# Kernel optimization log

Measured on AMD Instinct MI355X. Metric: run time of the kernel, lower is better.

Reference implementation:

```python
import jax, jax.numpy as jnp
from jax import lax
import numpy as np

N, T, D, H, HG, OG = 2048, 256, 16, 256, 256, 128

def setup_inputs() -> dict:
    key = jax.random.key(0)
    ks = jax.random.split(key, 16)
    s = 0.05
    return {
        'x':    jax.random.normal(ks[0], (N, T, D), jnp.float32),
        'Wih0': jax.random.normal(ks[1], (4 * H, D), jnp.float32) * s,
        'Whh0': jax.random.normal(ks[2], (4 * H, H), jnp.float32) * s,
        'bih0': jax.random.normal(ks[3], (4 * H,), jnp.float32) * s,
        'bhh0': jax.random.normal(ks[4], (4 * H,), jnp.float32) * s,
        'Wih1': jax.random.normal(ks[5], (4 * H, H), jnp.float32) * s,
        'Whh1': jax.random.normal(ks[6], (4 * H, H), jnp.float32) * s,
        'bih1': jax.random.normal(ks[7], (4 * H,), jnp.float32) * s,
        'bhh1': jax.random.normal(ks[8], (4 * H,), jnp.float32) * s,
        'Wg1':  jax.random.normal(ks[9], (H, HG), jnp.float32) * s,
        'Wg2':  jax.random.normal(ks[10], (HG, OG), jnp.float32) * s,
        'Wfc':  jax.random.normal(ks[11], (OG, 1), jnp.float32) * s,
        'bfc':  jax.random.normal(ks[12], (1,), jnp.float32) * s,
    }

def lstm_layer(x, Wih, Whh, bih, bhh):
    # x: [N, T, Din]; torch gate order i, f, g, o stacked along 4H
    n = x.shape[0]
    h4 = Whh.shape[0]
    hid = h4 // 4
    xg = jnp.einsum('ntd,gd->ntg', x, Wih) + bih + bhh  # precompute input part
    def step(carry, g_t):
        h, c = carry
        g = g_t + h @ Whh.T
        i, f, gg, o = jnp.split(g, 4, axis=-1)
        c = jax.nn.sigmoid(f) * c + jax.nn.sigmoid(i) * jnp.tanh(gg)
        h = jax.nn.sigmoid(o) * jnp.tanh(c)
        return (h, c), h
    h0 = jnp.zeros((n, hid), x.dtype)
    (_, _), hs = lax.scan(step, (h0, h0), jnp.swapaxes(xg, 0, 1))
    return jnp.swapaxes(hs, 0, 1)  # [N, T, H]

def adjacency(nf):
    # detached correlation graph + symmetric degree normalization
    f = lax.stop_gradient(nf)
    xc = f - f.mean(axis=1, keepdims=True)
    cov = xc @ xc.T
    d = jnp.sqrt(jnp.diag(cov))
    corr = jnp.nan_to_num(jnp.clip(cov / (d[:, None] * d[None, :]), -1.0, 1.0))
    A = corr + jnp.eye(f.shape[0], dtype=f.dtype)
    dinv = jnp.power(A.sum(axis=1), -0.5)
    dinv = jnp.where(jnp.isinf(dinv), 0.0, dinv)
    return dinv[:, None] * A * dinv[None, :]

def reference(x, Wih0, Whh0, bih0, bhh0, Wih1, Whh1, bih1, bhh1, Wg1, Wg2, Wfc, bfc):
    h = lstm_layer(x, Wih0, Whh0, bih0, bhh0)
    h = lstm_layer(h, Wih1, Whh1, bih1, bhh1)
    nf = h[:, -1, :]                      # [N, H]
    adj = adjacency(nf)                   # [N, N]
    g1 = jax.nn.relu(adj @ (nf @ Wg1))    # GCN layer 1 (dropout=0, eval)
    g2 = adj @ (g1 @ Wg2)                 # GCN layer 2
    pred = g2 @ Wfc + bfc                 # [N, 1]
    return pred[:, 0]
```

## Files before the change

### kernel.cpp

```cpp
#include <hip/hip_runtime.h>
#include <hip/hip_bf16.h>
#include <cmath>

#define NN 2048
#define TT 256
#define DD 16
#define HH 256
#define NBLK 512

typedef __attribute__((ext_vector_type(8))) short short8;
typedef __attribute__((ext_vector_type(4))) float f32x4;

__device__ __forceinline__ float sigmoidf_(float x){ return 1.0f/(1.0f+expf(-x)); }

__device__ __forceinline__ void glds16(const __hip_bfloat16* g, __hip_bfloat16* l){
  __builtin_amdgcn_global_load_lds(
      (const __attribute__((address_space(1))) void*)g,
      (__attribute__((address_space(3))) void*)l, 16, 0, 0);
}
__device__ __forceinline__ void glds16_dev(const __hip_bfloat16* g, __hip_bfloat16* l){
  __builtin_amdgcn_global_load_lds(
      (const __attribute__((address_space(1))) void*)g,
      (__attribute__((address_space(3))) void*)l, 16, 0, 17);
}

__global__ __launch_bounds__(256) void pack_w2(const float* __restrict__ W,
                                               __hip_bfloat16* __restrict__ P){
  int tid = blockIdx.x*256 + threadIdx.x;
  int r = tid >> 8, k = tid & 255;
  float w = W[tid];
  __hip_bfloat16 h = __float2bfloat16(w);
  __hip_bfloat16 l = __float2bfloat16(w - __bfloat162float(h));
  size_t base = (size_t)r*512;
  P[base + k] = h; P[base + 256 + k] = l;
}
__global__ __launch_bounds__(256) void pack_w0(const float* __restrict__ W,
                                               __hip_bfloat16* __restrict__ P){
  int tid = blockIdx.x*256 + threadIdx.x;
  int r = tid >> 4, k = tid & 15;
  float w = W[tid];
  __hip_bfloat16 h = __float2bfloat16(w);
  __hip_bfloat16 l = __float2bfloat16(w - __bfloat162float(h));
  size_t base = (size_t)r*64;
  P[base + k] = h; P[base + 16 + k] = h; P[base + 32 + k] = l;
  P[base + 48 + k] = __float2bfloat16(0.0f);
}
__global__ __launch_bounds__(256) void pack_x(const float* __restrict__ x,
                                              __hip_bfloat16* __restrict__ Xp){
  int tid = blockIdx.x*256 + threadIdx.x;
  const float* xr = x + (size_t)tid*16;
  __hip_bfloat16* o = Xp + (size_t)tid*64;
  for (int k=0;k<16;k++){
    float v = xr[k];
    __hip_bfloat16 h = __float2bfloat16(v);
    __hip_bfloat16 l = __float2bfloat16(v - __bfloat162float(h));
    o[k] = h; o[16+k] = l; o[32+k] = h; o[48+k] = __float2bfloat16(0.0f);
  }
}
__global__ __launch_bounds__(256) void recon_nf(const __hip_bfloat16* __restrict__ hi,
    const __hip_bfloat16* __restrict__ lo, float* __restrict__ nf){
  int tid = blockIdx.x*256 + threadIdx.x;
  nf[tid] = __bfloat162float(hi[tid]) + __bfloat162float(lo[tid]);
}

__global__ __launch_bounds__(256) void bar_init(unsigned* __restrict__ bar){
  for (int i = threadIdx.x; i < 2048; i += 256) bar[i] = 0u;
}

__device__ __forceinline__ void lean_sync(unsigned* bar, int t, int bid){
  __syncthreads();
  if (threadIdx.x == 0){
    const int x = bid & 7;
    unsigned a = __hip_atomic_fetch_add(bar + x*16, 1u, __ATOMIC_RELAXED,
                                        __HIP_MEMORY_SCOPE_AGENT);
    if (a == (unsigned)(64u*(t+1) - 1u)){
      unsigned g = __hip_atomic_fetch_add(bar + 128, 1u, __ATOMIC_RELAXED,
                                          __HIP_MEMORY_SCOPE_AGENT);
      if (g == (unsigned)(8u*(t+1) - 1u)){
        #pragma unroll
        for (int i=0;i<8;i++)
          __hip_atomic_store(bar + 1536 + i*64, (unsigned)(t+1),
                             __ATOMIC_RELAXED, __HIP_MEMORY_SCOPE_AGENT);
      } else {
        while (__hip_atomic_load(bar + 1536 + x*64, __ATOMIC_RELAXED,
                                 __HIP_MEMORY_SCOPE_AGENT) < (unsigned)(t+1))
          __builtin_amdgcn_s_sleep(4);
      }
    } else {
      while (__hip_atomic_load(bar + 1536 + x*64, __ATOMIC_RELAXED,
                               __HIP_MEMORY_SCOPE_AGENT) < (unsigned)(t+1))
        __builtin_amdgcn_s_sleep(4);
    }
  }
  __syncthreads();
}

__device__ __forceinline__ void mm_merged(
    const __hip_bfloat16* __restrict__ Ahi, const __hip_bfloat16* __restrict__ Alo,
    size_t lda,
    const __hip_bfloat16* __restrict__ Bhi, const __hip_bfloat16* __restrict__ Blo,
    size_t ldb, int Klen,
    int m0, int j0, int wv, int lane, int rr, int sw8, int frow,
    f32x4 (&acc)[2][4],
    __hip_bfloat16* AsH, __hip_bfloat16* AsL,
    __hip_bfloat16* BsH, __hip_bfloat16* BsL)
{
  const size_t arow = (size_t)(m0 + wv*32 + rr)*lda + sw8;
  const size_t brow = (size_t)(wv*256 + j0 + rr)*ldb + sw8;
  for (int kb=0; kb<Klen; kb+=64){
    {
      const __hip_bfloat16* AbH = Ahi + arow + kb;
      __hip_bfloat16* AdH = AsH + (wv*32)*64;
      #pragma unroll
      for (int c2=0;c2<4;c2++) glds16_dev(AbH + (size_t)(c2*8)*lda, AdH + c2*8*64);
      const __hip_bfloat16* AbL = Alo + arow + kb;
      __hip_bfloat16* AdL = AsL + (wv*32)*64;
      #pragma unroll
      for (int c2=0;c2<4;c2++) glds16_dev(AbL + (size_t)(c2*8)*lda, AdL + c2*8*64);
      const __hip_bfloat16* Bb1 = Bhi + brow + kb;
      __hip_bfloat16* Bd1 = BsH + (wv<<4)*64;
      glds16(Bb1, Bd1); glds16(Bb1 + (size_t)8*ldb, Bd1 + 8*64);
      const __hip_bfloat16* Bb2 = Blo + brow + kb;
      __hip_bfloat16* Bd2 = BsL + (wv<<4)*64;
      glds16(Bb2, Bd2); glds16(Bb2 + (size_t)8*ldb, Bd2 + 8*64);
    }
    __syncthreads();
    #pragma unroll
    for (int w2=0; w2<2; ++w2){
      const int sl8 = ((((w2<<2) + (lane>>4)) ^ (lane&7)) << 3);
      short8 ah0 = *(const short8*)&AsH[(wv*32 +      frow)*64 + sl8];
      short8 ah1 = *(const short8*)&AsH[(wv*32 + 16 + frow)*64 + sl8];
      short8 al0 = *(const short8*)&AsL[(wv*32 +      frow)*64 + sl8];
      short8 al1 = *(const short8*)&AsL[(wv*32 + 16 + frow)*64 + sl8];
      #pragma unroll
      for (int g=0; g<4; ++g){
        short8 bh = *(const short8*)&BsH[((g<<4) + frow)*64 + sl8];
        acc[0][g] = __builtin_amdgcn_mfma_f32_16x16x32_bf16(ah0, bh, acc[0][g], 0,0,0);
        acc[1][g] = __builtin_amdgcn_mfma_f32_16x16x32_bf16(ah1, bh, acc[1][g], 0,0,0);
        acc[0][g] = __builtin_amdgcn_mfma_f32_16x16x32_bf16(al0, bh, acc[0][g], 0,0,0);
        acc[1][g] = __builtin_amdgcn_mfma_f32_16x16x32_bf16(al1, bh, acc[1][g], 0,0,0);
        short8 bl = *(const short8*)&BsL[((g<<4) + frow)*64 + sl8];
        acc[0][g] = __builtin_amdgcn_mfma_f32_16x16x32_bf16(ah0, bl, acc[0][g], 0,0,0);
        acc[1][g] = __builtin_amdgcn_mfma_f32_16x16x32_bf16(ah1, bl, acc[1][g], 0,0,0);
      }
    }
    __syncthreads();
  }
}

__device__ __forceinline__ void mm_single64(
    const __hip_bfloat16* __restrict__ A, size_t lda,
    const __hip_bfloat16* __restrict__ B, size_t ldb,
    int m0, int j0, int wv, int lane, int rr, int sw8, int frow,
    f32x4 (&acc)[2][4],
    __hip_bfloat16* As0, __hip_bfloat16* Bh0)
{
  {
    const __hip_bfloat16* Ab = A + (size_t)(m0 + wv*32 + rr)*lda + sw8;
    __hip_bfloat16* Ad = As0 + (wv*32)*64;
    #pragma unroll
    for (int c2=0;c2<4;c2++) glds16(Ab + (size_t)(c2*8)*lda, Ad + c2*8*64);
    const __hip_bfloat16* Bb1 = B + (size_t)(wv*256 + j0 + rr)*ldb + sw8;
    __hip_bfloat16* Bd1 = Bh0 + (wv<<4)*64;
    glds16(Bb1, Bd1); glds16(Bb1 + (size_t)8*ldb, Bd1 + 8*64);
  }
  __syncthreads();
  #pragma unroll
  for (int w2=0; w2<2; ++w2){
    const int sl8 = ((((w2<<2) + (lane>>4)) ^ (lane&7)) << 3);
    short8 a0 = *(const short8*)&As0[(wv*32 +      frow)*64 + sl8];
    short8 a1 = *(const short8*)&As0[(wv*32 + 16 + frow)*64 + sl8];
    #pragma unroll
    for (int g=0; g<4; ++g){
      short8 b1 = *(const short8*)&Bh0[((g<<4) + frow)*64 + sl8];
      acc[0][g] = __builtin_amdgcn_mfma_f32_16x16x32_bf16(a0, b1, acc[0][g], 0,0,0);
      acc[1][g] = __builtin_amdgcn_mfma_f32_16x16x32_bf16(a1, b1, acc[1][g], 0,0,0);
    }
  }
  __syncthreads();
}

__global__ __launch_bounds__(256, 2) void lstm2_all(
    const __hip_bfloat16* __restrict__ Xp,
    const __hip_bfloat16* __restrict__ P0ih,
    const __hip_bfloat16* __restrict__ P0hh,
    const __hip_bfloat16* __restrict__ P1ih,
    const __hip_bfloat16* __restrict__ P1hh,
    const float* __restrict__ bih0, const float* __restrict__ bhh0,
    const float* __restrict__ bih1, const float* __restrict__ bhh1,
    __hip_bfloat16* __restrict__ H0hi0, __hip_bfloat16* __restrict__ H0lo0,
    __hip_bfloat16* __restrict__ H0hi1, __hip_bfloat16* __restrict__ H0lo1,
    __hip_bfloat16* __restrict__ H1hi0, __hip_bfloat16* __restrict__ H1lo0,
    __hip_bfloat16* __restrict__ H1hi1, __hip_bfloat16* __restrict__ H1lo1,
    unsigned* __restrict__ bar)
{
  __shared__ __align__(16) __hip_bfloat16 AsH[128*64];
  __shared__ __align__(16) __hip_bfloat16 AsL[128*64];
  __shared__ __align__(16) __hip_bfloat16 BsH[64*64];
  __shared__ __align__(16) __hip_bfloat16 BsL[64*64];

  const int bid = blockIdx.x;
  const int xcd = bid & 7;
  const int slot = bid >> 3;
  const bool isL0 = xcd < 4;
  const int lg = isL0 ? xcd : (xcd - 4);
  const int jg = ((lg & 1) << 3) + (slot & 7);
  const int mg = ((lg >> 1) << 3) + (slot >> 3);
  const int m0 = mg << 7;
  const int j0 = jg << 4;
  const int lane = threadIdx.x & 63, wv = threadIdx.x >> 6;
  const int rr = lane >> 3;
  const int sw8 = (((lane & 7) ^ rr) << 3);
  const int frow = lane & 15;
  const int odd = frow & 1;

  const int j = j0 + frow;
  const float* bih = isL0 ? bih0 : bih1;
  const float* bhh = isL0 ? bhh0 : bhh1;
  const float b0 = bih[j]        + bhh[j];
  const float b1 = bih[HH + j]   + bhh[HH + j];
  const float b2 = bih[2*HH + j] + bhh[2*HH + j];
  const float b3 = bih[3*HH + j] + bhh[3*HH + j];

  float creg[2][4] = {{0.f,0.f,0.f,0.f},{0.f,0.f,0.f,0.f}};

  for (int t = 0; t <= TT; ++t){
    const int p = t & 1;
    const bool active = isL0 ? (t < TT) : (t >= 1);
    if (active){
      f32x4 acc[2][4] = {};
      const __hip_bfloat16* h0p_hi = p ? H0hi0 : H0hi1;
      const __hip_bfloat16* h0p_lo = p ? H0lo0 : H0lo1;
      if (isL0){
        if (t != 0){
          mm_merged(h0p_hi, h0p_lo, 256, P0hh, P0hh+256, 512, 256,
                    m0, j0, wv, lane, rr, sw8, frow, acc, AsH, AsL, BsH, BsL);
        }
        mm_single64(Xp + (size_t)t*64, (size_t)TT*64, P0ih, 64,
                    m0, j0, wv, lane, rr, sw8, frow, acc, AsH, BsH);
      } else {
        mm_merged(h0p_hi, h0p_lo, 256, P1ih, P1ih+256, 512, 256,
                  m0, j0, wv, lane, rr, sw8, frow, acc, AsH, AsL, BsH, BsL);
        if (t != 1){
          const __hip_bfloat16* h1p_hi = p ? H1hi1 : H1hi0;
          const __hip_bfloat16* h1p_lo = p ? H1lo1 : H1lo0;
          mm_merged(h1p_hi, h1p_lo, 256, P1hh, P1hh+256, 512, 256,
                    m0, j0, wv, lane, rr, sw8, frow, acc, AsH, AsL, BsH, BsL);
        }
      }
      __hip_bfloat16* ohi = isL0 ? (p ? H0hi1 : H0hi0)
                                 : (p ? H1hi0 : H1hi1);
      __hip_bfloat16* olo = isL0 ? (p ? H0lo1 : H0lo0)
                                 : (p ? H1lo0 : H1lo1);
      #pragma unroll
      for (int mt=0; mt<2; ++mt){
        const int mrb = m0 + wv*32 + mt*16 + ((lane>>4)<<2);
        #pragma unroll
        for (int r=0; r<4; ++r){
          float gi = acc[mt][0][r] + b0;
          float gf = acc[mt][1][r] + b1;
          float gg = acc[mt][2][r] + b2;
          float go = acc[mt][3][r] + b3;
          float cn = sigmoidf_(gf)*creg[mt][r] + sigmoidf_(gi)*tanhf(gg);
          creg[mt][r] = cn;
          float hv = sigmoidf_(go)*tanhf(cn);
          __hip_bfloat16 hb = __float2bfloat16(hv);
          __hip_bfloat16 lb = __float2bfloat16(hv - __bfloat162float(hb));
          unsigned hs = (unsigned)*reinterpret_cast<unsigned short*>(&hb);
          unsigned ls = (unsigned)*reinterpret_cast<unsigned short*>(&lb);
          unsigned hp = (unsigned)__shfl_xor((int)hs, 1);
          unsigned lp = (unsigned)__shfl_xor((int)ls, 1);
          const size_t base = (size_t)(mrb + r)*HH + (size_t)(j & ~1);
          if (!odd){
            unsigned v = hs | (hp << 16);
            __hip_atomic_store((unsigned*)(ohi + base), v,
                               __ATOMIC_RELAXED, __HIP_MEMORY_SCOPE_AGENT);
          } else {
            unsigned v = lp | (ls << 16);
            __hip_atomic_store((unsigned*)(olo + base), v,
                               __ATOMIC_RELAXED, __HIP_MEMORY_SCOPE_AGENT);
          }
        }
      }
    }
    if (t < TT) lean_sync(bar, t, bid);
  }
}

__global__ __launch_bounds__(256) void gemm_nn(
    float* __restrict__ C, const float* __restrict__ A, const float* __restrict__ B,
    int K, int lda, int ldb, int ldc, int relu)
{
  __shared__ float As_[16][68];
  __shared__ float Bs_[16][64];
  float acc[4][4] = {};
  const int tx = threadIdx.x;
  const int m0 = blockIdx.y<<6, n0 = blockIdx.x<<6;
  const int am = tx>>2, ak = (tx&3)<<2;
  const int bk = tx>>4, bn = (tx&15)<<2;
  const int mm = (tx>>4)<<2, nc = (tx&15)<<2;
  for (int kb=0; kb<K; kb+=16){
    float4 av = *reinterpret_cast<const float4*>(A + (size_t)(m0+am)*lda + kb + ak);
    As_[ak][am]=av.x; As_[ak+1][am]=av.y; As_[ak+2][am]=av.z; As_[ak+3][am]=av.w;
    *reinterpret_cast<float4*>(&Bs_[bk][bn]) =
      *reinterpret_cast<const float4*>(B + (size_t)(kb+bk)*ldb + n0 + bn);
    __syncthreads();
    #pragma unroll
    for (int k=0;k<16;k++){
      float4 a4 = *reinterpret_cast<const float4*>(&As_[k][mm]);
      float4 b4 = *reinterpret_cast<const float4*>(&Bs_[k][nc]);
      acc[0][0]=fmaf(a4.x,b4.x,acc[0][0]); acc[0][1]=fmaf(a4.x,b4.y,acc[0][1]);
      acc[0][2]=fmaf(a4.x,b4.z,acc[0][2]); acc[0][3]=fmaf(a4.x,b4.w,acc[0][3]);
      acc[1][0]=fmaf(a4.y,b4.x,acc[1][0]); acc[1][1]=fmaf(a4.y,b4.y,acc[1][1]);
      acc[1][2]=fmaf(a4.y,b4.z,acc[1][2]); acc[1][3]=fmaf(a4.y,b4.w,acc[1][3]);
      acc[2][0]=fmaf(a4.z,b4.x,acc[2][0]); acc[2][1]=fmaf(a4.z,b4.y,acc[2][1]);
      acc[2][2]=fmaf(a4.z,b4.z,acc[2][2]); acc[2][3]=fmaf(a4.z,b4.w,acc[2][3]);
      acc[3][0]=fmaf(a4.w,b4.x,acc[3][0]); acc[3][1]=fmaf(a4.w,b4.y,acc[3][1]);
      acc[3][2]=fmaf(a4.w,b4.z,acc[3][2]); acc[3][3]=fmaf(a4.w,b4.w,acc[3][3]);
    }
    __syncthreads();
  }
  #pragma unroll
  for (int r=0;r<4;r++){
    float4 v = make_float4(acc[r][0],acc[r][1],acc[r][2],acc[r][3]);
    if (relu){ v.x=fmaxf(v.x,0.f); v.y=fmaxf(v.y,0.f); v.z=fmaxf(v.z,0.f); v.w=fmaxf(v.w,0.f); }
    *reinterpret_cast<float4*>(C + (size_t)(m0+mm+r)*ldc + n0 + nc) = v;
  }
}

__global__ __launch_bounds__(256) void gemm_nt(
    float* __restrict__ C, const float* __restrict__ A, const float* __restrict__ B,
    int K, int lda, int ldb, int ldc)
{
  __shared__ float As_[16][68];
  __shared__ float Bs_[16][68];
  float acc[4][4] = {};
  const int tx = threadIdx.x;
  const int m0 = blockIdx.y<<6, n0 = blockIdx.x<<6;
  const int am = tx>>2, ak = (tx&3)<<2;
  const int mm = (tx>>4)<<2, nc = (tx&15)<<2;
  for (int kb=0; kb<K; kb+=16){
    float4 av = *reinterpret_cast<const float4*>(A + (size_t)(m0+am)*lda + kb + ak);
    As_[ak][am]=av.x; As_[ak+1][am]=av.y; As_[ak+2][am]=av.z; As_[ak+3][am]=av.w;
    float4 bv = *reinterpret_cast<const float4*>(B + (size_t)(n0+am)*ldb + kb + ak);
    Bs_[ak][am]=bv.x; Bs_[ak+1][am]=bv.y; Bs_[ak+2][am]=bv.z; Bs_[ak+3][am]=bv.w;
    __syncthreads();
    #pragma unroll
    for (int k=0;k<16;k++){
      float4 a4 = *reinterpret_cast<const float4*>(&As_[k][mm]);
      float4 b4 = *reinterpret_cast<const float4*>(&Bs_[k][nc]);
      acc[0][0]=fmaf(a4.x,b4.x,acc[0][0]); acc[0][1]=fmaf(a4.x,b4.y,acc[0][1]);
      acc[0][2]=fmaf(a4.x,b4.z,acc[0][2]); acc[0][3]=fmaf(a4.x,b4.w,acc[0][3]);
      acc[1][0]=fmaf(a4.y,b4.x,acc[1][0]); acc[1][1]=fmaf(a4.y,b4.y,acc[1][1]);
      acc[1][2]=fmaf(a4.y,b4.z,acc[1][2]); acc[1][3]=fmaf(a4.y,b4.w,acc[1][3]);
      acc[2][0]=fmaf(a4.z,b4.x,acc[2][0]); acc[2][1]=fmaf(a4.z,b4.y,acc[2][1]);
      acc[2][2]=fmaf(a4.z,b4.z,acc[2][2]); acc[2][3]=fmaf(a4.z,b4.w,acc[2][3]);
      acc[3][0]=fmaf(a4.w,b4.x,acc[3][0]); acc[3][1]=fmaf(a4.w,b4.y,acc[3][1]);
      acc[3][2]=fmaf(a4.w,b4.z,acc[3][2]); acc[3][3]=fmaf(a4.w,b4.w,acc[3][3]);
    }
    __syncthreads();
  }
  #pragma unroll
  for (int r=0;r<4;r++){
    float4 v = make_float4(acc[r][0],acc[r][1],acc[r][2],acc[r][3]);
    *reinterpret_cast<float4*>(C + (size_t)(m0+mm+r)*ldc + n0 + nc) = v;
  }
}

__global__ __launch_bounds__(256) void rowstat(const float* __restrict__ nf,
    float* __restrict__ xc, float* __restrict__ dvec)
{
  __shared__ float red[256];
  int n = blockIdx.x, tx = threadIdx.x;
  float v = nf[(size_t)n*HH + tx];
  red[tx] = v; __syncthreads();
  for (int s=128; s>0; s>>=1){ if (tx<s) red[tx]+=red[tx+s]; __syncthreads(); }
  float mean = red[0] * (1.0f/HH);
  __syncthreads();
  float d = v - mean;
  xc[(size_t)n*HH + tx] = d;
  red[tx] = d*d; __syncthreads();
  for (int s=128; s>0; s>>=1){ if (tx<s) red[tx]+=red[tx+s]; __syncthreads(); }
  if (tx==0) dvec[n] = sqrtf(red[0]);
}

__global__ __launch_bounds__(256) void rowsum(const float* __restrict__ cov,
    const float* __restrict__ dvec, float* __restrict__ dinv)
{
  __shared__ float red[256];
  int i = blockIdx.x, tx = threadIdx.x;
  float di = dvec[i];
  float s = 0.f;
  for (int jj=tx; jj<NN; jj+=256){
    float r = cov[(size_t)i*NN + jj] / (di * dvec[jj]);
    if (r != r) r = 0.f; else r = fminf(1.f, fmaxf(-1.f, r));
    s += r;
  }
  red[tx]=s; __syncthreads();
  for (int st=128; st>0; st>>=1){ if (tx<st) red[tx]+=red[tx+st]; __syncthreads(); }
  if (tx==0){
    float tot = red[0] + 1.0f;
    float p = powf(tot, -0.5f);
    if (isinf(p)) p = 0.f;
    dinv[i] = p;
  }
}

__global__ __launch_bounds__(256) void adjnorm(float* __restrict__ cov,
    const float* __restrict__ dvec, const float* __restrict__ dinv)
{
  size_t idx = (size_t)blockIdx.x*256 + threadIdx.x;
  int i = (int)(idx >> 11), jj = (int)(idx & (NN-1));
  float r = cov[idx] / (dvec[i]*dvec[jj]);
  if (r != r) r = 0.f; else r = fminf(1.f, fmaxf(-1.f, r));
  if (i==jj) r += 1.f;
  cov[idx] = dinv[i]*r*dinv[jj];
}

__global__ __launch_bounds__(128) void predk(const float* __restrict__ G2,
    const float* __restrict__ Wfc, const float* __restrict__ bfc, float* __restrict__ out)
{
  int n = blockIdx.x, tx = threadIdx.x;
  float v = G2[(size_t)n*128 + tx] * Wfc[tx];
  for (int off=32; off>0; off>>=1) v += __shfl_down(v, off);
  __shared__ float p[2];
  if ((tx&63)==0) p[tx>>6] = v;
  __syncthreads();
  if (tx==0) out[n] = p[0] + p[1] + bfc[0];
}

extern "C" void kernel_launch(void* const* d_in, const int* in_sizes, int n_in,
                              void* d_out, int out_size, void* d_ws, size_t ws_size,
                              hipStream_t stream)
{
  const float* x    = (const float*)d_in[0];
  const float* Wih0 = (const float*)d_in[1];
  const float* Whh0 = (const float*)d_in[2];
  const float* bih0 = (const float*)d_in[3];
  const float* bhh0 = (const float*)d_in[4];
  const float* Wih1 = (const float*)d_in[5];
  const float* Whh1 = (const float*)d_in[6];
  const float* bih1 = (const float*)d_in[7];
  const float* bhh1 = (const float*)d_in[8];
  const float* Wg1  = (const float*)d_in[9];
  const float* Wg2  = (const float*)d_in[10];
  const float* Wfc  = (const float*)d_in[11];
  const float* bfc  = (const float*)d_in[12];
  float* out = (float*)d_out;

  char* w = (char*)d_ws;
  auto alloc = [&](size_t bytes){ char* p = w; w += (bytes + 255) & ~(size_t)255; return p; };
  __hip_bfloat16* Xp   = (__hip_bfloat16*)alloc((size_t)NN*TT*64*2);
  __hip_bfloat16* P0hh = (__hip_bfloat16*)alloc((size_t)1024*512*2);
  __hip_bfloat16* P1ih = (__hip_bfloat16*)alloc((size_t)1024*512*2);
  __hip_bfloat16* P1hh = (__hip_bfloat16*)alloc((size_t)1024*512*2);
  __hip_bfloat16* P0ih = (__hip_bfloat16*)alloc((size_t)1024*64*2);
  __hip_bfloat16 *H0hi[2], *H0lo[2], *H1hi[2], *H1lo[2];
  for (int i=0;i<2;i++){ H0hi[i]=(__hip_bfloat16*)alloc((size_t)NN*HH*2);
                         H0lo[i]=(__hip_bfloat16*)alloc((size_t)NN*HH*2); }
  for (int i=0;i<2;i++){ H1hi[i]=(__hip_bfloat16*)alloc((size_t)NN*HH*2);
                         H1lo[i]=(__hip_bfloat16*)alloc((size_t)NN*HH*2); }
  float* nf   = (float*)alloc((size_t)NN*HH*4);
  float* xc   = (float*)alloc((size_t)NN*HH*4);
  float* cov  = (float*)alloc((size_t)NN*NN*4);
  float* t1   = (float*)alloc((size_t)NN*HH*4);
  float* G1   = (float*)alloc((size_t)NN*HH*4);
  float* t2   = (float*)alloc((size_t)NN*128*4);
  float* G2   = (float*)alloc((size_t)NN*128*4);
  float* dvec = (float*)alloc((size_t)NN*4);
  float* dinv = (float*)alloc((size_t)NN*4);
  unsigned* bar = (unsigned*)alloc(8192);

  hipLaunchKernelGGL(bar_init, dim3(1), dim3(256), 0, stream, bar);
  hipLaunchKernelGGL(pack_w2, dim3(1024), dim3(256), 0, stream, Whh0, P0hh);
  hipLaunchKernelGGL(pack_w2, dim3(1024), dim3(256), 0, stream, Wih1, P1ih);
  hipLaunchKernelGGL(pack_w2, dim3(1024), dim3(256), 0, stream, Whh1, P1hh);
  hipLaunchKernelGGL(pack_w0, dim3(64),   dim3(256), 0, stream, Wih0, P0ih);
  hipLaunchKernelGGL(pack_x,  dim3(2048), dim3(256), 0, stream, x, Xp);

  hipLaunchKernelGGL(lstm2_all, dim3(NBLK), dim3(256), 0, stream,
      Xp, P0ih, P0hh, P1ih, P1hh, bih0, bhh0, bih1, bhh1,
      H0hi[0], H0lo[0], H0hi[1], H0lo[1],
      H1hi[0], H1lo[0], H1hi[1], H1lo[1], bar);

  hipLaunchKernelGGL(recon_nf, dim3(2048), dim3(256), 0, stream, H1hi[1], H1lo[1], nf);

  hipLaunchKernelGGL(rowstat, dim3(NN), dim3(256), 0, stream, nf, xc, dvec);
  hipLaunchKernelGGL(gemm_nt, dim3(NN/64, NN/64), dim3(256), 0, stream,
      cov, xc, xc, HH, HH, HH, NN);
  hipLaunchKernelGGL(rowsum, dim3(NN), dim3(256), 0, stream, cov, dvec, dinv);
  hipLaunchKernelGGL(adjnorm, dim3(NN*NN/256), dim3(256), 0, stream, cov, dvec, dinv);

  hipLaunchKernelGGL(gemm_nn, dim3(HH/64, NN/64), dim3(256), 0, stream,
      t1, nf, Wg1, HH, HH, HH, HH, 0);
  hipLaunchKernelGGL(gemm_nn, dim3(HH/64, NN/64), dim3(256), 0, stream,
      G1, cov, t1, NN, NN, HH, HH, 1);
  hipLaunchKernelGGL(gemm_nn, dim3(128/64, NN/64), dim3(256), 0, stream,
      t2, G1, Wg2, HH, HH, 128, 128, 0);
  hipLaunchKernelGGL(gemm_nn, dim3(128/64, NN/64), dim3(256), 0, stream,
      G2, cov, t2, NN, NN, 128, 128, 0);
  hipLaunchKernelGGL(predk, dim3(NN), dim3(128), 0, stream, G2, Wfc, bfc, out);
}
```

Measured before the change: 4.648 ms.

## Repartition persistent LSTM kernel across 768 blocks with unequal layer tiles

The persistent two-layer LSTM kernel now launches 768 blocks at three per CU instead of 512 at two. Layer-1 blocks, which do two recurrent GEMMs per step, get half the rows of layer-0 blocks so per-step work is more even across the grid barrier. Tiles change from 128 rows × 16 gate columns to 64 or 32 rows × 32 gate columns, so weight slices double while activation slices shrink. The grid barrier threshold is raised to match, and the extra co-resident blocks risk more register and LDS pressure and more barrier traffic.

```diff
diff --git a/kernel.cpp b/kernel.cpp
--- a/kernel.cpp
+++ b/kernel.cpp
@@ -6,7 +6,7 @@
 #define TT 256
 #define DD 16
 #define HH 256
-#define NBLK 512
+#define NBLK 768
 
 typedef __attribute__((ext_vector_type(8))) short short8;
 typedef __attribute__((ext_vector_type(4))) float f32x4;
@@ -73,7 +73,7 @@
     const int x = bid & 7;
     unsigned a = __hip_atomic_fetch_add(bar + x*16, 1u, __ATOMIC_RELAXED,
                                         __HIP_MEMORY_SCOPE_AGENT);
-    if (a == (unsigned)(64u*(t+1) - 1u)){
+    if (a == (unsigned)(96u*(t+1) - 1u)){
       unsigned g = __hip_atomic_fetch_add(bar + 128, 1u, __ATOMIC_RELAXED,
                                           __HIP_MEMORY_SCOPE_AGENT);
       if (g == (unsigned)(8u*(t+1) - 1u)){
@@ -95,92 +95,7 @@
   __syncthreads();
 }
 
-__device__ __forceinline__ void mm_merged(
-    const __hip_bfloat16* __restrict__ Ahi, const __hip_bfloat16* __restrict__ Alo,
-    size_t lda,
-    const __hip_bfloat16* __restrict__ Bhi, const __hip_bfloat16* __restrict__ Blo,
-    size_t ldb, int Klen,
-    int m0, int j0, int wv, int lane, int rr, int sw8, int frow,
-    f32x4 (&acc)[2][4],
-    __hip_bfloat16* AsH, __hip_bfloat16* AsL,
-    __hip_bfloat16* BsH, __hip_bfloat16* BsL)
-{
-  const size_t arow = (size_t)(m0 + wv*32 + rr)*lda + sw8;
-  const size_t brow = (size_t)(wv*256 + j0 + rr)*ldb + sw8;
-  for (int kb=0; kb<Klen; kb+=64){
-    {
-      const __hip_bfloat16* AbH = Ahi + arow + kb;
-      __hip_bfloat16* AdH = AsH + (wv*32)*64;
-      #pragma unroll
-      for (int c2=0;c2<4;c2++) glds16_dev(AbH + (size_t)(c2*8)*lda, AdH + c2*8*64);
-      const __hip_bfloat16* AbL = Alo + arow + kb;
-      __hip_bfloat16* AdL = AsL + (wv*32)*64;
-      #pragma unroll
-      for (int c2=0;c2<4;c2++) glds16_dev(AbL + (size_t)(c2*8)*lda, AdL + c2*8*64);
-      const __hip_bfloat16* Bb1 = Bhi + brow + kb;
-      __hip_bfloat16* Bd1 = BsH + (wv<<4)*64;
-      glds16(Bb1, Bd1); glds16(Bb1 + (size_t)8*ldb, Bd1 + 8*64);
-      const __hip_bfloat16* Bb2 = Blo + brow + kb;
-      __hip_bfloat16* Bd2 = BsL + (wv<<4)*64;
-      glds16(Bb2, Bd2); glds16(Bb2 + (size_t)8*ldb, Bd2 + 8*64);
-    }
-    __syncthreads();
-    #pragma unroll
-    for (int w2=0; w2<2; ++w2){
-      const int sl8 = ((((w2<<2) + (lane>>4)) ^ (lane&7)) << 3);
-      short8 ah0 = *(const short8*)&AsH[(wv*32 +      frow)*64 + sl8];
-      short8 ah1 = *(const short8*)&AsH[(wv*32 + 16 + frow)*64 + sl8];
-      short8 al0 = *(const short8*)&AsL[(wv*32 +      frow)*64 + sl8];
-      short8 al1 = *(const short8*)&AsL[(wv*32 + 16 + frow)*64 + sl8];
-      #pragma unroll
-      for (int g=0; g<4; ++g){
-        short8 bh = *(const short8*)&BsH[((g<<4) + frow)*64 + sl8];
-        acc[0][g] = __builtin_amdgcn_mfma_f32_16x16x32_bf16(ah0, bh, acc[0][g], 0,0,0);
-        acc[1][g] = __builtin_amdgcn_mfma_f32_16x16x32_bf16(ah1, bh, acc[1][g], 0,0,0);
-        acc[0][g] = __builtin_amdgcn_mfma_f32_16x16x32_bf16(al0, bh, acc[0][g], 0,0,0);
-        acc[1][g] = __builtin_amdgcn_mfma_f32_16x16x32_bf16(al1, bh, acc[1][g], 0,0,0);
-        short8 bl = *(const short8*)&BsL[((g<<4) + frow)*64 + sl8];
-        acc[0][g] = __builtin_amdgcn_mfma_f32_16x16x32_bf16(ah0, bl, acc[0][g], 0,0,0);
-        acc[1][g] = __builtin_amdgcn_mfma_f32_16x16x32_bf16(ah1, bl, acc[1][g], 0,0,0);
-      }
-    }
-    __syncthreads();
-  }
-}
-
-__device__ __forceinline__ void mm_single64(
-    const __hip_bfloat16* __restrict__ A, size_t lda,
-    const __hip_bfloat16* __restrict__ B, size_t ldb,
-    int m0, int j0, int wv, int lane, int rr, int sw8, int frow,
-    f32x4 (&acc)[2][4],
-    __hip_bfloat16* As0, __hip_bfloat16* Bh0)
-{
-  {
-    const __hip_bfloat16* Ab = A + (size_t)(m0 + wv*32 + rr)*lda + sw8;
-    __hip_bfloat16* Ad = As0 + (wv*32)*64;
-    #pragma unroll
-    for (int c2=0;c2<4;c2++) glds16(Ab + (size_t)(c2*8)*lda, Ad + c2*8*64);
-    const __hip_bfloat16* Bb1 = B + (size_t)(wv*256 + j0 + rr)*ldb + sw8;
-    __hip_bfloat16* Bd1 = Bh0 + (wv<<4)*64;
-    glds16(Bb1, Bd1); glds16(Bb1 + (size_t)8*ldb, Bd1 + 8*64);
-  }
-  __syncthreads();
-  #pragma unroll
-  for (int w2=0; w2<2; ++w2){
-    const int sl8 = ((((w2<<2) + (lane>>4)) ^ (lane&7)) << 3);
-    short8 a0 = *(const short8*)&As0[(wv*32 +      frow)*64 + sl8];
-    short8 a1 = *(const short8*)&As0[(wv*32 + 16 + frow)*64 + sl8];
-    #pragma unroll
-    for (int g=0; g<4; ++g){
-      short8 b1 = *(const short8*)&Bh0[((g<<4) + frow)*64 + sl8];
-      acc[0][g] = __builtin_amdgcn_mfma_f32_16x16x32_bf16(a0, b1, acc[0][g], 0,0,0);
-      acc[1][g] = __builtin_amdgcn_mfma_f32_16x16x32_bf16(a1, b1, acc[1][g], 0,0,0);
-    }
-  }
-  __syncthreads();
-}
-
-__global__ __launch_bounds__(256, 2) void lstm2_all(
+__global__ __launch_bounds__(256, 3) void lstm2_all(
     const __hip_bfloat16* __restrict__ Xp,
     const __hip_bfloat16* __restrict__ P0ih,
     const __hip_bfloat16* __restrict__ P0hh,
@@ -194,75 +109,184 @@
     __hip_bfloat16* __restrict__ H1hi1, __hip_bfloat16* __restrict__ H1lo1,
     unsigned* __restrict__ bar)
 {
-  __shared__ __align__(16) __hip_bfloat16 AsH[128*64];
-  __shared__ __align__(16) __hip_bfloat16 AsL[128*64];
-  __shared__ __align__(16) __hip_bfloat16 BsH[64*64];
-  __shared__ __align__(16) __hip_bfloat16 BsL[64*64];
+  __shared__ __align__(16) __hip_bfloat16 AsH[64*64];
+  __shared__ __align__(16) __hip_bfloat16 AsL[64*64];
+  __shared__ __align__(16) __hip_bfloat16 BsH[128*64];
+  __shared__ __align__(16) __hip_bfloat16 BsL[128*64];
 
   const int bid = blockIdx.x;
   const int xcd = bid & 7;
   const int slot = bid >> 3;
-  const bool isL0 = xcd < 4;
-  const int lg = isL0 ? xcd : (xcd - 4);
-  const int jg = ((lg & 1) << 3) + (slot & 7);
-  const int mg = ((lg >> 1) << 3) + (slot >> 3);
-  const int m0 = mg << 7;
-  const int j0 = jg << 4;
+  const bool isL0 = slot < 32;
+  const int s = isL0 ? slot : (slot - 32);
+  const int m0 = xcd*256 + (isL0 ? ((s>>3)<<6) : ((s>>3)<<5));
+  const int j0 = (s & 7) << 5;
   const int lane = threadIdx.x & 63, wv = threadIdx.x >> 6;
   const int rr = lane >> 3;
   const int sw8 = (((lane & 7) ^ rr) << 3);
   const int frow = lane & 15;
   const int odd = frow & 1;
-
-  const int j = j0 + frow;
-  const float* bih = isL0 ? bih0 : bih1;
-  const float* bhh = isL0 ? bhh0 : bhh1;
-  const float b0 = bih[j]        + bhh[j];
-  const float b1 = bih[HH + j]   + bhh[HH + j];
-  const float b2 = bih[2*HH + j] + bhh[2*HH + j];
-  const float b3 = bih[3*HH + j] + bhh[3*HH + j];
+  const int jsub = wv & 1;
+  const int wmb = isL0 ? ((wv>>1)<<5) : ((wv>>1)<<4);
+  const int nms = isL0 ? 2 : 1;
+
+  const int j = j0 + (jsub<<4) + frow;
+  const float* bihp = isL0 ? bih0 : bih1;
+  const float* bhhp = isL0 ? bhh0 : bhh1;
+  const float b0 = bihp[j]        + bhhp[j];
+  const float b1 = bihp[HH + j]   + bhhp[HH + j];
+  const float b2 = bihp[2*HH + j] + bhhp[2*HH + j];
+  const float b3 = bihp[3*HH + j] + bhhp[3*HH + j];
 
   float creg[2][4] = {{0.f,0.f,0.f,0.f},{0.f,0.f,0.f,0.f}};
+
+  const size_t aW0 = (size_t)(m0 + wv*16 + rr)*256 + sw8;
+  const size_t aW1 = (size_t)(m0 + wv*8  + rr)*256 + sw8;
+  const size_t bW  = (size_t)(wv*256 + j0 + rr)*512 + sw8;
+  const size_t bxW = (size_t)(wv*256 + j0 + rr)*64  + sw8;
 
   for (int t = 0; t <= TT; ++t){
     const int p = t & 1;
     const bool active = isL0 ? (t < TT) : (t >= 1);
     if (active){
       f32x4 acc[2][4] = {};
-      const __hip_bfloat16* h0p_hi = p ? H0hi0 : H0hi1;
-      const __hip_bfloat16* h0p_lo = p ? H0lo0 : H0lo1;
       if (isL0){
         if (t != 0){
-          mm_merged(h0p_hi, h0p_lo, 256, P0hh, P0hh+256, 512, 256,
-                    m0, j0, wv, lane, rr, sw8, frow, acc, AsH, AsL, BsH, BsL);
+          const __hip_bfloat16* hh = p ? H0hi0 : H0hi1;
+          const __hip_bfloat16* hl = p ? H0lo0 : H0lo1;
+          for (int kb=0; kb<256; kb+=64){
+            glds16_dev(hh + aW0 + kb,                 AsH + (wv*16)*64);
+            glds16_dev(hh + aW0 + (size_t)8*256 + kb, AsH + (wv*16+8)*64);
+            glds16_dev(hl + aW0 + kb,                 AsL + (wv*16)*64);
+            glds16_dev(hl + aW0 + (size_t)8*256 + kb, AsL + (wv*16+8)*64);
+            #pragma unroll
+            for (int c2=0;c2<4;c2++){
+              glds16(P0hh + bW + (size_t)(c2*8)*512 + kb,       BsH + (wv*32 + c2*8)*64);
+              glds16(P0hh + 256 + bW + (size_t)(c2*8)*512 + kb, BsL + (wv*32 + c2*8)*64);
+            }
+            __syncthreads();
+            #pragma unroll
+            for (int w2=0; w2<2; ++w2){
+              const int sl8 = ((((w2<<2) + (lane>>4)) ^ (lane&7)) << 3);
+              #pragma unroll
+              for (int ms=0; ms<2; ++ms){
+                short8 ah = *(const short8*)&AsH[(wmb + ms*16 + frow)*64 + sl8];
+                short8 al = *(const short8*)&AsL[(wmb + ms*16 + frow)*64 + sl8];
+                #pragma unroll
+                for (int g=0; g<4; ++g){
+                  const int brow = (g*32 + (jsub<<4) + frow)*64 + sl8;
+                  short8 bh = *(const short8*)&BsH[brow];
+                  acc[ms][g] = __builtin_amdgcn_mfma_f32_16x16x32_bf16(ah, bh, acc[ms][g], 0,0,0);
+                  acc[ms][g] = __builtin_amdgcn_mfma_f32_16x16x32_bf16(al, bh, acc[ms][g], 0,0,0);
+                  short8 bl = *(const short8*)&BsL[brow];
+                  acc[ms][g] = __builtin_amdgcn_mfma_f32_16x16x32_bf16(ah, bl, acc[ms][g], 0,0,0);
+                }
+              }
+            }
+            __syncthreads();
+          }
         }
-        mm_single64(Xp + (size_t)t*64, (size_t)TT*64, P0ih, 64,
-                    m0, j0, wv, lane, rr, sw8, frow, acc, AsH, BsH);
+        {
+          const size_t axW = (size_t)(m0 + wv*16 + rr)*((size_t)TT*64)
+                           + (size_t)t*64 + sw8;
+          glds16(Xp + axW,                       AsH + (wv*16)*64);
+          glds16(Xp + axW + (size_t)8*TT*64,     AsH + (wv*16+8)*64);
+          #pragma unroll
+          for (int c2=0;c2<4;c2++)
+            glds16(P0ih + bxW + (size_t)(c2*8)*64, BsH + (wv*32 + c2*8)*64);
+          __syncthreads();
+          #pragma unroll
+          for (int w2=0; w2<2; ++w2){
+            const int sl8 = ((((w2<<2) + (lane>>4)) ^ (lane&7)) << 3);
+            #pragma unroll
+            for (int ms=0; ms<2; ++ms){
+              short8 a0 = *(const short8*)&AsH[(wmb + ms*16 + frow)*64 + sl8];
+              #pragma unroll
+              for (int g=0; g<4; ++g){
+                short8 b1v = *(const short8*)&BsH[(g*32 + (jsub<<4) + frow)*64 + sl8];
+                acc[ms][g] = __builtin_amdgcn_mfma_f32_16x16x32_bf16(a0, b1v, acc[ms][g], 0,0,0);
+              }
+            }
+          }
+          __syncthreads();
+        }
       } else {
-        mm_merged(h0p_hi, h0p_lo, 256, P1ih, P1ih+256, 512, 256,
-                  m0, j0, wv, lane, rr, sw8, frow, acc, AsH, AsL, BsH, BsL);
-        if (t != 1){
-          const __hip_bfloat16* h1p_hi = p ? H1hi1 : H1hi0;
-          const __hip_bfloat16* h1p_lo = p ? H1lo1 : H1lo0;
-          mm_merged(h1p_hi, h1p_lo, 256, P1hh, P1hh+256, 512, 256,
-                    m0, j0, wv, lane, rr, sw8, frow, acc, AsH, AsL, BsH, BsL);
+        const __hip_bfloat16* h0h = p ? H0hi0 : H0hi1;
+        const __hip_bfloat16* h0l = p ? H0lo0 : H0lo1;
+        for (int kb=0; kb<256; kb+=64){
+          glds16_dev(h0h + aW1 + kb, AsH + (wv*8)*64);
+          glds16_dev(h0l + aW1 + kb, AsL + (wv*8)*64);
+          #pragma unroll
+          for (int c2=0;c2<4;c2++){
+            glds16(P1ih + bW + (size_t)(c2*8)*512 + kb,       BsH + (wv*32 + c2*8)*64);
+            glds16(P1ih + 256 + bW + (size_t)(c2*8)*512 + kb, BsL + (wv*32 + c2*8)*64);
+          }
+          __syncthreads();
+          #pragma unroll
+          for (int w2=0; w2<2; ++w2){
+            const int sl8 = ((((w2<<2) + (lane>>4)) ^ (lane&7)) << 3);
+            short8 ah = *(const short8*)&AsH[(wmb + frow)*64 + sl8];
+            short8 al = *(const short8*)&AsL[(wmb + frow)*64 + sl8];
+            #pragma unroll
+            for (int g=0; g<4; ++g){
+              const int brow = (g*32 + (jsub<<4) + frow)*64 + sl8;
+              short8 bh = *(const short8*)&BsH[brow];
+              acc[0][g] = __builtin_amdgcn_mfma_f32_16x16x32_bf16(ah, bh, acc[0][g], 0,0,0);
+              acc[0][g] = __builtin_amdgcn_mfma_f32_16x16x32_bf16(al, bh, acc[0][g], 0,0,0);
+              short8 bl = *(const short8*)&BsL[brow];
+              acc[0][g] = __builtin_amdgcn_mfma_f32_16x16x32_bf16(ah, bl, acc[0][g], 0,0,0);
+            }
+          }
+          __syncthreads();
+        }
+        if (t >= 2){
+          const __hip_bfloat16* h1h = p ? H1hi1 : H1hi0;
+          const __hip_bfloat16* h1l = p ? H1lo1 : H1lo0;
+          for (int kb=0; kb<256; kb+=64){
+            glds16_dev(h1h + aW1 + kb, AsH + (wv*8)*64);
+            glds16_dev(h1l + aW1 + kb, AsL + (wv*8)*64);
+            #pragma unroll
+            for (int c2=0;c2<4;c2++){
+              glds16(P1hh + bW + (size_t)(c2*8)*512 + kb,       BsH + (wv*32 + c2*8)*64);
+              glds16(P1hh + 256 + bW + (size_t)(c2*8)*512 + kb, BsL + (wv*32 + c2*8)*64);
+            }
+            __syncthreads();
+            #pragma unroll
+            for (int w2=0; w2<2; ++w2){
+              const int sl8 = ((((w2<<2) + (lane>>4)) ^ (lane&7)) << 3);
+              short8 ah = *(const short8*)&AsH[(wmb + frow)*64 + sl8];
+              short8 al = *(const short8*)&AsL[(wmb + frow)*64 + sl8];
+              #pragma unroll
+              for (int g=0; g<4; ++g){
+                const int brow = (g*32 + (jsub<<4) + frow)*64 + sl8;
+                short8 bh = *(const short8*)&BsH[brow];
+                acc[0][g] = __builtin_amdgcn_mfma_f32_16x16x32_bf16(ah, bh, acc[0][g], 0,0,0);
+                acc[0][g] = __builtin_amdgcn_mfma_f32_16x16x32_bf16(al, bh, acc[0][g], 0,0,0);
+                short8 bl = *(const short8*)&BsL[brow];
+                acc[0][g] = __builtin_amdgcn_mfma_f32_16x16x32_bf16(ah, bl, acc[0][g], 0,0,0);
+              }
+            }
+            __syncthreads();
+          }
         }
       }
+
       __hip_bfloat16* ohi = isL0 ? (p ? H0hi1 : H0hi0)
                                  : (p ? H1hi0 : H1hi1);
       __hip_bfloat16* olo = isL0 ? (p ? H0lo1 : H0lo0)
                                  : (p ? H1lo0 : H1lo1);
-      #pragma unroll
-      for (int mt=0; mt<2; ++mt){
-        const int mrb = m0 + wv*32 + mt*16 + ((lane>>4)<<2);
+      float* cr = creg[0];
+      for (int ms=0; ms<nms; ++ms){
+        const int mrb = m0 + wmb + ms*16 + ((lane>>4)<<2);
+        float* cm = (ms==0) ? creg[0] : creg[1];
         #pragma unroll
         for (int r=0; r<4; ++r){
-          float gi = acc[mt][0][r] + b0;
-          float gf = acc[mt][1][r] + b1;
-          float gg = acc[mt][2][r] + b2;
-          float go = acc[mt][3][r] + b3;
-          float cn = sigmoidf_(gf)*creg[mt][r] + sigmoidf_(gi)*tanhf(gg);
-          creg[mt][r] = cn;
+          float gi = acc[ms][0][r] + b0;
+          float gf = acc[ms][1][r] + b1;
+          float gg = acc[ms][2][r] + b2;
+          float go = acc[ms][3][r] + b3;
+          float cn = sigmoidf_(gf)*cm[r] + sigmoidf_(gi)*tanhf(gg);
+          cm[r] = cn;
           float hv = sigmoidf_(go)*tanhf(cn);
           __hip_bfloat16 hb = __float2bfloat16(hv);
           __hip_bfloat16 lb = __float2bfloat16(hv - __bfloat162float(hb));
@@ -282,6 +306,7 @@
           }
         }
       }
+      (void)cr;
     }
     if (t < TT) lean_sync(bar, t, bid);
   }
```

Result: slower. 8.573 ms (+84.4%).
